# Kernel tuning notes

Measured on AMD Instinct MI355X. Metric: run time of the kernel, lower is better.

The kernel has to match this reference:

```python
import jax, jax.numpy as jnp
import numpy as np

U, I, H, E = 50000, 50000, 128, 800000


def segment_softmax(vals, seg, num):
    m = jax.ops.segment_max(vals, seg, num_segments=num)
    ex = jnp.exp(vals - m[seg])
    s = jax.ops.segment_sum(ex, seg, num_segments=num)
    return ex / s[seg]


def setup_inputs() -> dict:
    key = jax.random.key(0)
    ks = jax.random.split(key, 16)
    scale = 1.0 / np.sqrt(H)
    inp = {
        "u_emb": jax.random.normal(ks[0], (U, H), jnp.float32),
        "i_emb": jax.random.normal(ks[1], (I, H), jnp.float32),
        "pVui": jax.random.normal(ks[2], (E, H), jnp.float32),
        "pKiu": jax.random.normal(ks[3], (E, H), jnp.float32),
        "w1": jax.random.normal(ks[4], (H, H), jnp.float32) * scale,
        "w2": jax.random.normal(ks[5], (H, H), jnp.float32) * scale,
        "w1b": jax.random.normal(ks[6], (H, H), jnp.float32) * scale,
        "w2b": jax.random.normal(ks[7], (H, H), jnp.float32) * scale,
        "w3": jax.random.normal(ks[8], (H, H), jnp.float32) * scale,
        "w4": jax.random.normal(ks[9], (H, H), jnp.float32) * scale,
        "edge_index": jax.random.randint(ks[10], (2, E), 0, min(U, I), jnp.int64),
        "last_u": jax.random.randint(ks[11], (2, U), 0, I, jnp.int64),
        "last_i": jax.random.randint(ks[12], (2, I), 0, U, jnp.int64),
        "graph": jnp.zeros((1,), jnp.int64),
    }
    return inp


def reference(u_emb, i_emb, pVui, pKiu, w1, w2, w1b, w2b, w3, w4,
              edge_index, last_u, last_i, graph):
    sqrt_d = np.sqrt(float(u_emb.shape[1])).astype if False else float(np.sqrt(u_emb.shape[1]))
    nu, ni = u_emb.shape[0], i_emb.shape[0]
    src_u, dst_i = edge_index[0], edge_index[1]  # per-edge (user, item)

    # ---- longterm ----
    um_att = u_emb @ w2.T            # [U,H]
    im_att = i_emb @ w1.T            # [I,H]
    # sparse_dense_mul(edge_index, um_att @ im_att.T) -> per-edge dot products
    e_vals = jnp.sum(um_att[src_u] * im_att[dst_i], axis=-1)  # [E]
    e_ui = e_vals + jnp.sum(um_att[src_u] * pVui, axis=-1)
    alphas = segment_softmax(e_ui / sqrt_d, src_u, nu)        # softmax over items per user
    e_iu = e_vals + jnp.sum(im_att[dst_i] * pKiu, axis=-1)
    betas = segment_softmax(e_iu / sqrt_d, dst_i, ni)         # softmax over users per item
    um_b = u_emb @ w2b.T
    im_b = i_emb @ w1b.T
    hLu = jax.ops.segment_sum(alphas[:, None] * (im_b[dst_i] + pKiu), src_u, num_segments=nu)
    hLi = jax.ops.segment_sum(betas[:, None] * (um_b[src_u] + pVui), dst_i, num_segments=ni)

    # ---- shortterm ----
    last_item = i_emb[last_u[1]] @ w3.T   # [U,H] last item embedding per user
    last_user = u_emb[last_i[1]] @ w4.T   # [I,H] last user embedding per item
    a_vals = jnp.sum(last_item[src_u] * im_att[dst_i], axis=-1)
    s_alphas = segment_softmax(a_vals / sqrt_d, src_u, nu)
    b_vals = jnp.sum(last_user[src_u] * im_att[dst_i], axis=-1)
    s_betas = segment_softmax(b_vals / sqrt_d, dst_i, ni)
    # pass_messages with p = ones -> messages + 1
    hSu = jax.ops.segment_sum(s_alphas[:, None] * (im_att[dst_i] + 1.0), src_u, num_segments=nu)
    hSi = jax.ops.segment_sum(s_betas[:, None] * (um_att[src_u] + 1.0), dst_i, num_segments=ni)
    return (hLu, hSu, hLi, hSi)
```

## Files before the change

kernel.cpp:

```cpp
#include <hip/hip_runtime.h>
#include <hip/hip_bf16.h>
#include <math.h>


#define WB 1024

typedef float fvec4 __attribute__((ext_vector_type(4)));

__device__ __forceinline__ float4 nt_load4(const float* p) {
    fvec4 v = __builtin_nontemporal_load((const fvec4*)p);
    return make_float4(v.x, v.y, v.z, v.w);
}
__device__ __forceinline__ float dot4(float4 a, float4 b) {
    return a.x * b.x + a.y * b.y + a.z * b.z + a.w * b.w;
}

struct Gemm6Desc {
    const float* X[6];
    const float* W[6];
    float*       O[6];
    const int*   g[6];
    int          ostride[6];
    int          nrows[6];
};

__global__ __launch_bounds__(256) void gemm6_kernel(Gemm6Desc d)
{
    __shared__ float Xl[64 * 32];
    __shared__ float Wl[128 * 32];
    const int j6 = blockIdx.y;
    const float* __restrict__ X = d.X[j6];
    const float* __restrict__ W = d.W[j6];
    float* __restrict__ O       = d.O[j6];
    const int* __restrict__ gidx = d.g[j6];
    const int ostride = d.ostride[j6];
    const int nrows   = d.nrows[j6];

    const int t  = threadIdx.x;
    const int tx = t & 15;
    const int ty = t >> 4;
    const int brow = blockIdx.x * 64;
    if (brow >= nrows) return;

    float acc[4][8];
#pragma unroll
    for (int j = 0; j < 4; ++j)
#pragma unroll
        for (int i = 0; i < 8; ++i) acc[j][i] = 0.f;

    for (int k0 = 0; k0 < 128; k0 += 32) {
        __syncthreads();
#pragma unroll
        for (int u = 0; u < 2; ++u) {
            int idx4 = t + u * 256;
            int r  = idx4 >> 3;
            int k4 = idx4 & 7;
            int row = brow + r;
            float4 v = make_float4(0.f, 0.f, 0.f, 0.f);
            if (row < nrows) {
                int g = gidx ? gidx[row] : row;
                v = *(const float4*)(X + (size_t)g * 128 + k0 + k4 * 4);
            }
            int sw = k4 ^ ((r >> 3) & 7);
            *(float4*)(Xl + r * 32 + sw * 4) = v;
        }
#pragma unroll
        for (int u = 0; u < 4; ++u) {
            int idx4 = t + u * 256;
            int c  = idx4 >> 3;
            int k4 = idx4 & 7;
            float4 v = *(const float4*)(W + (size_t)c * 128 + k0 + k4 * 4);
            int sw = k4 ^ ((c >> 3) & 7);
            *(float4*)(Wl + c * 32 + sw * 4) = v;
        }
        __syncthreads();
#pragma unroll
        for (int k4 = 0; k4 < 8; ++k4) {
            float4 xv[4], wv[8];
#pragma unroll
            for (int j = 0; j < 4; ++j) {
                int r = ty * 4 + j;
                xv[j] = *(const float4*)(Xl + r * 32 + ((k4 ^ ((r >> 3) & 7)) * 4));
            }
#pragma unroll
            for (int i = 0; i < 8; ++i) {
                int c = tx * 8 + i;
                wv[i] = *(const float4*)(Wl + c * 32 + ((k4 ^ ((c >> 3) & 7)) * 4));
            }
#pragma unroll
            for (int j = 0; j < 4; ++j)
#pragma unroll
                for (int i = 0; i < 8; ++i) {
                    acc[j][i] += xv[j].x * wv[i].x;
                    acc[j][i] += xv[j].y * wv[i].y;
                    acc[j][i] += xv[j].z * wv[i].z;
                    acc[j][i] += xv[j].w * wv[i].w;
                }
        }
    }
#pragma unroll
    for (int j = 0; j < 4; ++j) {
        int row = brow + ty * 4 + j;
        if (row < nrows) {
            float* op = O + (size_t)row * ostride + tx * 8;
            *(float4*)(op)     = make_float4(acc[j][0], acc[j][1], acc[j][2], acc[j][3]);
            *(float4*)(op + 4) = make_float4(acc[j][4], acc[j][5], acc[j][6], acc[j][7]);
        }
    }
}

__global__ __launch_bounds__(256) void hist_kernel(
    const int* __restrict__ ei, int E,
    int* __restrict__ deg_u, int* __restrict__ deg_i)
{
    int e = blockIdx.x * 256 + threadIdx.x;
    if (e < E) {
        atomicAdd(&deg_u[ei[e]], 1);
        atomicAdd(&deg_i[ei[E + e]], 1);
    }
}

__global__ __launch_bounds__(256) void scan_blocksums_kernel(
    const int* __restrict__ deg_u, int nu, int nbu,
    const int* __restrict__ deg_i, int ni,
    int* __restrict__ bsum)
{
    int b = blockIdx.x;
    const int* deg; int n; int base;
    if (b < nbu) { deg = deg_u; n = nu; base = b * WB; }
    else         { deg = deg_i; n = ni; base = (b - nbu) * WB; }
    int t = threadIdx.x;
    int s = 0;
#pragma unroll
    for (int j = 0; j < 4; ++j) {
        int i = base + t * 4 + j;
        if (i < n) s += deg[i];
    }
#pragma unroll
    for (int o = 32; o > 0; o >>= 1) s += __shfl_xor(s, o);
    __shared__ int wt[4];
    if ((t & 63) == 0) wt[t >> 6] = s;
    __syncthreads();
    if (t == 0) bsum[b] = wt[0] + wt[1] + wt[2] + wt[3];
}

__global__ void scan_partials_kernel(
    const int* __restrict__ bsum, int* __restrict__ bscan,
    int nbu, int nbi,
    int* __restrict__ off_u, int nu, int* __restrict__ off_i, int ni)
{
    if (threadIdx.x != 0) return;
    if (blockIdx.x == 0) {
        int c = 0;
        for (int b = 0; b < nbu; ++b) { bscan[b] = c; c += bsum[b]; }
        off_u[nu] = c;
    } else {
        int c = 0;
        for (int b = 0; b < nbi; ++b) { bscan[nbu + b] = c; c += bsum[nbu + b]; }
        off_i[ni] = c;
    }
}

__global__ __launch_bounds__(256) void scan_final_kernel(
    const int* __restrict__ deg_u, int nu, int nbu,
    const int* __restrict__ deg_i, int ni,
    const int* __restrict__ bscan,
    int* __restrict__ off_u, int* __restrict__ cur_u,
    int* __restrict__ off_i, int* __restrict__ cur_i)
{
    int b = blockIdx.x;
    const int* deg; int n; int base; int* off; int* cur;
    if (b < nbu) { deg = deg_u; n = nu; base = b * WB; off = off_u; cur = cur_u; }
    else         { deg = deg_i; n = ni; base = (b - nbu) * WB; off = off_i; cur = cur_i; }
    int t = threadIdx.x;
    int lane = t & 63, w = t >> 6;
    int v[4];
    int s = 0;
#pragma unroll
    for (int j = 0; j < 4; ++j) {
        int i = base + t * 4 + j;
        v[j] = (i < n) ? deg[i] : 0;
        s += v[j];
    }
    int inc = s;
#pragma unroll
    for (int o = 1; o < 64; o <<= 1) {
        int x = __shfl_up(inc, o);
        if (lane >= o) inc += x;
    }
    int excl = inc - s;
    __shared__ int wt[4];
    if (lane == 63) wt[w] = inc;
    __syncthreads();
    int wbase = 0;
    for (int j = 0; j < w; ++j) wbase += wt[j];
    int e = bscan[b] + wbase + excl;
#pragma unroll
    for (int j = 0; j < 4; ++j) {
        int i = base + t * 4 + j;
        if (i < n) { off[i] = e; cur[i] = e; }
        e += v[j];
    }
}

__global__ __launch_bounds__(256) void scatter_ids_kernel(
    const int* __restrict__ ei, int E,
    int* __restrict__ cur_u, int* __restrict__ cur_i,
    int2* __restrict__ eu_list, int2* __restrict__ ei_list)
{
    int e = blockIdx.x * 256 + threadIdx.x;
    if (e < E) {
        int u = ei[e], v = ei[E + e];
        int pu = atomicAdd(&cur_u[u], 1);
        eu_list[pu] = make_int2(v, e);
        int pi = atomicAdd(&cur_i[v], 1);
        ei_list[pi] = make_int2(u, e);
    }
}

__global__ __launch_bounds__(256) void gather_u_kernel(
    const float* __restrict__ fusedU,
    const float* __restrict__ fusedI,
    const float* __restrict__ last_item, const float* __restrict__ last_user,
    const float* __restrict__ pVui, const float* __restrict__ pKiu,
    const int2* __restrict__ lst,
    const int* __restrict__ off_u,
    float2* __restrict__ x24,
    float* __restrict__ hLu, float* __restrict__ hSu, int U, float inv_sqrt_d)
{
    const int wid  = (int)(((size_t)blockIdx.x * blockDim.x + threadIdx.x) >> 6);
    const int lane = threadIdx.x & 63;
    if (wid >= U) return;
    const int g = lane >> 4;
    const int q = lane & 15;

    const float4* fu4 = (const float4*)(fusedU    + (size_t)wid * 256);
    const float4* li4 = (const float4*)(last_item + (size_t)wid * 128);
    const float4* lu4 = (const float4*)(last_user + (size_t)wid * 128);
    const float4 um0 = fu4[q],      um1 = fu4[q + 16];
    const float4 li0 = li4[q],      li1 = li4[q + 16];
    const float4 lu0 = lu4[q],      lu1 = lu4[q + 16];

    float4 a1l = make_float4(0.f,0.f,0.f,0.f), a1h = make_float4(0.f,0.f,0.f,0.f);
    float4 a3l = make_float4(0.f,0.f,0.f,0.f), a3h = make_float4(0.f,0.f,0.f,0.f);
    float s1 = 0.f, s3 = 0.f;
    const int e0 = off_u[wid], e1 = off_u[wid + 1];

    int eA = e0 + g, eB = eA + 4;
    bool vA = eA < e1, vB = eB < e1;
    int2 rA = vA ? lst[eA] : make_int2(0, 0);
    int2 rB = vB ? lst[eB] : rA;

    while (vA) {
        int eA2 = eA + 8, eB2 = eB + 8;
        bool vA2 = eA2 < e1, vB2 = eB2 < e1;
        int2 rA2 = vA2 ? lst[eA2] : make_int2(0, 0);
        int2 rB2 = vB2 ? lst[eB2] : rA2;

        const float4* fIA = (const float4*)(fusedI + (size_t)rA.x * 256);
        const float*  pvA = pVui + (size_t)rA.y * 128;
        const float*  pkA = pKiu + (size_t)rA.y * 128;
        const float4* fIB = (const float4*)(fusedI + (size_t)rB.x * 256);
        const float*  pvB = pVui + (size_t)rB.y * 128;
        const float*  pkB = pKiu + (size_t)rB.y * 128;

        float4 iaA0 = fIA[q],      iaA1 = fIA[q + 16];
        float4 ibA0 = fIA[32 + q], ibA1 = fIA[48 + q];
        float4 pvA0 = nt_load4(pvA + q * 4), pvA1 = nt_load4(pvA + 64 + q * 4);
        float4 pkA0 = nt_load4(pkA + q * 4), pkA1 = nt_load4(pkA + 64 + q * 4);
        float4 iaB0 = fIB[q],      iaB1 = fIB[q + 16];
        float4 ibB0 = fIB[32 + q], ibB1 = fIB[48 + q];
        float4 pvB0 = nt_load4(pvB + q * 4), pvB1 = nt_load4(pvB + 64 + q * 4);
        float4 pkB0 = nt_load4(pkB + q * 4), pkB1 = nt_load4(pkB + 64 + q * 4);

        float pA0 = dot4(um0, iaA0) + dot4(um1, iaA1);
        float qA1 = pA0 + dot4(um0, pvA0) + dot4(um1, pvA1);
        float qA2 = pA0 + dot4(iaA0, pkA0) + dot4(iaA1, pkA1);
        float qA3 = dot4(li0, iaA0) + dot4(li1, iaA1);
        float qA4 = dot4(lu0, iaA0) + dot4(lu1, iaA1);
        float pB0 = dot4(um0, iaB0) + dot4(um1, iaB1);
        float qB1 = pB0 + dot4(um0, pvB0) + dot4(um1, pvB1);
        float qB2 = pB0 + dot4(iaB0, pkB0) + dot4(iaB1, pkB1);
        float qB3 = dot4(li0, iaB0) + dot4(li1, iaB1);
        float qB4 = dot4(lu0, iaB0) + dot4(lu1, iaB1);
#pragma unroll
        for (int o = 8; o > 0; o >>= 1) {
            qA1 += __shfl_xor(qA1, o); qA2 += __shfl_xor(qA2, o);
            qA3 += __shfl_xor(qA3, o); qA4 += __shfl_xor(qA4, o);
            qB1 += __shfl_xor(qB1, o); qB2 += __shfl_xor(qB2, o);
            qB3 += __shfl_xor(qB3, o); qB4 += __shfl_xor(qB4, o);
        }
        float x1A = __expf(qA1 * inv_sqrt_d);
        float x2A = __expf(qA2 * inv_sqrt_d);
        float x3A = __expf(qA3 * inv_sqrt_d);
        float x4A = __expf(qA4 * inv_sqrt_d);
        float mB  = vB ? 1.f : 0.f;
        float x1B = __expf(qB1 * inv_sqrt_d) * mB;
        float x2B = __expf(qB2 * inv_sqrt_d);
        float x3B = __expf(qB3 * inv_sqrt_d) * mB;
        float x4B = __expf(qB4 * inv_sqrt_d);

        a1l.x += x1A*(ibA0.x+pkA0.x) + x1B*(ibB0.x+pkB0.x);
        a1l.y += x1A*(ibA0.y+pkA0.y) + x1B*(ibB0.y+pkB0.y);
        a1l.z += x1A*(ibA0.z+pkA0.z) + x1B*(ibB0.z+pkB0.z);
        a1l.w += x1A*(ibA0.w+pkA0.w) + x1B*(ibB0.w+pkB0.w);
        a1h.x += x1A*(ibA1.x+pkA1.x) + x1B*(ibB1.x+pkB1.x);
        a1h.y += x1A*(ibA1.y+pkA1.y) + x1B*(ibB1.y+pkB1.y);
        a1h.z += x1A*(ibA1.z+pkA1.z) + x1B*(ibB1.z+pkB1.z);
        a1h.w += x1A*(ibA1.w+pkA1.w) + x1B*(ibB1.w+pkB1.w);
        a3l.x += x3A*(iaA0.x+1.f) + x3B*(iaB0.x+1.f);
        a3l.y += x3A*(iaA0.y+1.f) + x3B*(iaB0.y+1.f);
        a3l.z += x3A*(iaA0.z+1.f) + x3B*(iaB0.z+1.f);
        a3l.w += x3A*(iaA0.w+1.f) + x3B*(iaB0.w+1.f);
        a3h.x += x3A*(iaA1.x+1.f) + x3B*(iaB1.x+1.f);
        a3h.y += x3A*(iaA1.y+1.f) + x3B*(iaB1.y+1.f);
        a3h.z += x3A*(iaA1.z+1.f) + x3B*(iaB1.z+1.f);
        a3h.w += x3A*(iaA1.w+1.f) + x3B*(iaB1.w+1.f);
        s1 += x1A + x1B; s3 += x3A + x3B;
        if (q == 0) {
            x24[rA.y] = make_float2(x2A, x4A);
            if (vB) x24[rB.y] = make_float2(x2B, x4B);
        }
        eA = eA2; eB = eB2; vA = vA2; vB = vB2; rA = rA2; rB = rB2;
    }
#pragma unroll
    for (int o = 16; o <= 32; o <<= 1) {
        a1l.x += __shfl_xor(a1l.x, o); a1l.y += __shfl_xor(a1l.y, o);
        a1l.z += __shfl_xor(a1l.z, o); a1l.w += __shfl_xor(a1l.w, o);
        a1h.x += __shfl_xor(a1h.x, o); a1h.y += __shfl_xor(a1h.y, o);
        a1h.z += __shfl_xor(a1h.z, o); a1h.w += __shfl_xor(a1h.w, o);
        a3l.x += __shfl_xor(a3l.x, o); a3l.y += __shfl_xor(a3l.y, o);
        a3l.z += __shfl_xor(a3l.z, o); a3l.w += __shfl_xor(a3l.w, o);
        a3h.x += __shfl_xor(a3h.x, o); a3h.y += __shfl_xor(a3h.y, o);
        a3h.z += __shfl_xor(a3h.z, o); a3h.w += __shfl_xor(a3h.w, o);
        s1 += __shfl_xor(s1, o);       s3 += __shfl_xor(s3, o);
    }
    if (lane < 16) {
        float r1 = (s1 > 0.f) ? 1.f / s1 : 0.f;
        float r3 = (s3 > 0.f) ? 1.f / s3 : 0.f;
        float4* oL = (float4*)(hLu + (size_t)wid * 128);
        float4* oS = (float4*)(hSu + (size_t)wid * 128);
        oL[q]      = make_float4(a1l.x*r1, a1l.y*r1, a1l.z*r1, a1l.w*r1);
        oL[q + 16] = make_float4(a1h.x*r1, a1h.y*r1, a1h.z*r1, a1h.w*r1);
        oS[q]      = make_float4(a3l.x*r3, a3l.y*r3, a3l.z*r3, a3l.w*r3);
        oS[q + 16] = make_float4(a3h.x*r3, a3h.y*r3, a3h.z*r3, a3h.w*r3);
    }
}

__global__ __launch_bounds__(256) void gather_i_kernel(
    const float* __restrict__ fusedU,
    const float* __restrict__ pVui,
    const int2* __restrict__ lst,
    const int* __restrict__ off_i,
    const float2* __restrict__ x24,
    float* __restrict__ hLi, float* __restrict__ hSi, int I)
{
    const int wid  = (int)(((size_t)blockIdx.x * blockDim.x + threadIdx.x) >> 6);
    const int lane = threadIdx.x & 63;
    if (wid >= I) return;
    const int g = lane >> 4;
    const int q = lane & 15;

    float4 a2l = make_float4(0.f,0.f,0.f,0.f), a2h = make_float4(0.f,0.f,0.f,0.f);
    float4 a4l = make_float4(0.f,0.f,0.f,0.f), a4h = make_float4(0.f,0.f,0.f,0.f);
    float s2 = 0.f, s4 = 0.f;
    const int e0 = off_i[wid], e1 = off_i[wid + 1];

    int eA = e0 + g, eB = eA + 4;
    bool vA = eA < e1, vB = eB < e1;
    int2 rA = vA ? lst[eA] : make_int2(0, 0);
    int2 rB = vB ? lst[eB] : rA;

    while (vA) {
        int eA2 = eA + 8, eB2 = eB + 8;
        bool vA2 = eA2 < e1, vB2 = eB2 < e1;
        int2 rA2 = vA2 ? lst[eA2] : make_int2(0, 0);
        int2 rB2 = vB2 ? lst[eB2] : rA2;

        const float4* fUA = (const float4*)(fusedU + (size_t)rA.x * 256);
        const float*  pvA = pVui + (size_t)rA.y * 128;
        const float4* fUB = (const float4*)(fusedU + (size_t)rB.x * 256);
        const float*  pvB = pVui + (size_t)rB.y * 128;

        float2 xA = x24[rA.y];
        float2 xB = x24[rB.y];
        float4 uaA0 = fUA[q],      uaA1 = fUA[q + 16];
        float4 ubA0 = fUA[32 + q], ubA1 = fUA[48 + q];
        float4 pvA0 = nt_load4(pvA + q * 4), pvA1 = nt_load4(pvA + 64 + q * 4);
        float4 uaB0 = fUB[q],      uaB1 = fUB[q + 16];
        float4 ubB0 = fUB[32 + q], ubB1 = fUB[48 + q];
        float4 pvB0 = nt_load4(pvB + q * 4), pvB1 = nt_load4(pvB + 64 + q * 4);

        if (!vB) { xB.x = 0.f; xB.y = 0.f; }
        a2l.x += xA.x*(ubA0.x+pvA0.x) + xB.x*(ubB0.x+pvB0.x);
        a2l.y += xA.x*(ubA0.y+pvA0.y) + xB.x*(ubB0.y+pvB0.y);
        a2l.z += xA.x*(ubA0.z+pvA0.z) + xB.x*(ubB0.z+pvB0.z);
        a2l.w += xA.x*(ubA0.w+pvA0.w) + xB.x*(ubB0.w+pvB0.w);
        a2h.x += xA.x*(ubA1.x+pvA1.x) + xB.x*(ubB1.x+pvB1.x);
        a2h.y += xA.x*(ubA1.y+pvA1.y) + xB.x*(ubB1.y+pvB1.y);
        a2h.z += xA.x*(ubA1.z+pvA1.z) + xB.x*(ubB1.z+pvB1.z);
        a2h.w += xA.x*(ubA1.w+pvA1.w) + xB.x*(ubB1.w+pvB1.w);
        a4l.x += xA.y*(uaA0.x+1.f) + xB.y*(uaB0.x+1.f);
        a4l.y += xA.y*(uaA0.y+1.f) + xB.y*(uaB0.y+1.f);
        a4l.z += xA.y*(uaA0.z+1.f) + xB.y*(uaB0.z+1.f);
        a4l.w += xA.y*(uaA0.w+1.f) + xB.y*(uaB0.w+1.f);
        a4h.x += xA.y*(uaA1.x+1.f) + xB.y*(uaB1.x+1.f);
        a4h.y += xA.y*(uaA1.y+1.f) + xB.y*(uaB1.y+1.f);
        a4h.z += xA.y*(uaA1.z+1.f) + xB.y*(uaB1.z+1.f);
        a4h.w += xA.y*(uaA1.w+1.f) + xB.y*(uaB1.w+1.f);
        s2 += xA.x + xB.x; s4 += xA.y + xB.y;

        eA = eA2; eB = eB2; vA = vA2; vB = vB2; rA = rA2; rB = rB2;
    }
#pragma unroll
    for (int o = 16; o <= 32; o <<= 1) {
        a2l.x += __shfl_xor(a2l.x, o); a2l.y += __shfl_xor(a2l.y, o);
        a2l.z += __shfl_xor(a2l.z, o); a2l.w += __shfl_xor(a2l.w, o);
        a2h.x += __shfl_xor(a2h.x, o); a2h.y += __shfl_xor(a2h.y, o);
        a2h.z += __shfl_xor(a2h.z, o); a2h.w += __shfl_xor(a2h.w, o);
        a4l.x += __shfl_xor(a4l.x, o); a4l.y += __shfl_xor(a4l.y, o);
        a4l.z += __shfl_xor(a4l.z, o); a4l.w += __shfl_xor(a4l.w, o);
        a4h.x += __shfl_xor(a4h.x, o); a4h.y += __shfl_xor(a4h.y, o);
        a4h.z += __shfl_xor(a4h.w - a4h.w + a4h.z, o); a4h.w += __shfl_xor(a4h.w, o);
        s2 += __shfl_xor(s2, o);       s4 += __shfl_xor(s4, o);
    }
    if (lane < 16) {
        float r2 = (s2 > 0.f) ? 1.f / s2 : 0.f;
        float r4 = (s4 > 0.f) ? 1.f / s4 : 0.f;
        float4* oL = (float4*)(hLi + (size_t)wid * 128);
        float4* oS = (float4*)(hSi + (size_t)wid * 128);
        oL[q]      = make_float4(a2l.x*r2, a2l.y*r2, a2l.z*r2, a2l.w*r2);
        oL[q + 16] = make_float4(a2h.x*r2, a2h.y*r2, a2h.z*r2, a2h.w*r2);
        oS[q]      = make_float4(a4l.x*r4, a4l.y*r4, a4l.z*r4, a4l.w*r4);
        oS[q + 16] = make_float4(a4h.x*r4, a4h.y*r4, a4h.z*r4, a4h.w*r4);
    }
}

extern "C" void kernel_launch(void* const* d_in, const int* in_sizes, int n_in,
                              void* d_out, int out_size, void* d_ws, size_t ws_size,
                              hipStream_t stream)
{
    const float* u_emb = (const float*)d_in[0];
    const float* i_emb = (const float*)d_in[1];
    const float* pVui  = (const float*)d_in[2];
    const float* pKiu  = (const float*)d_in[3];
    const float* w1    = (const float*)d_in[4];
    const float* w2    = (const float*)d_in[5];
    const float* w1b   = (const float*)d_in[6];
    const float* w2b   = (const float*)d_in[7];
    const float* w3    = (const float*)d_in[8];
    const float* w4    = (const float*)d_in[9];
    const int* edge_index = (const int*)d_in[10];
    const int* last_u     = (const int*)d_in[11];
    const int* last_i     = (const int*)d_in[12];

    const int U = in_sizes[0] / 128;
    const int I = in_sizes[1] / 128;
    const int E = in_sizes[10] / 2;
    const int nbu = (U + WB - 1) / WB;
    const int nbi = (I + WB - 1) / WB;

    float* ws = (float*)d_ws;
    float* fusedU    = ws;  ws += (size_t)U * 256;
    float* fusedI    = ws;  ws += (size_t)I * 256;
    float* last_item = ws;  ws += (size_t)U * 128;
    float* last_user = ws;  ws += (size_t)I * 128;
    float2* x24 = (float2*)ws;  ws += (size_t)E * 2;
    int2* eu_list = (int2*)ws;  ws += (size_t)E * 2;
    int2* ei_list = (int2*)ws;  ws += (size_t)E * 2;
    int* ip = (int*)ws;
    int* deg_u   = ip;  ip += U;
    int* deg_i   = ip;  ip += I;
    int* off_u   = ip;  ip += U + 1;
    int* off_i   = ip;  ip += I + 1;
    int* cur_u   = ip;  ip += U;
    int* cur_i   = ip;  ip += I;
    int* bsum    = ip;  ip += nbu + nbi;
    int* bscan   = ip;  ip += nbu + nbi;

    float* hLu = (float*)d_out;
    float* hSu = hLu + (size_t)U * 128;
    float* hLi = hSu + (size_t)U * 128;
    float* hSi = hLi + (size_t)I * 128;

    hipMemsetAsync(deg_u, 0, (size_t)(U + I) * sizeof(int), stream);

    dim3 blk(256);
    const int eblk = (E + 255) / 256;
    hist_kernel<<<eblk, blk, 0, stream>>>(edge_index, E, deg_u, deg_i);
    scan_blocksums_kernel<<<nbu + nbi, blk, 0, stream>>>(deg_u, U, nbu, deg_i, I, bsum);
    scan_partials_kernel<<<2, 64, 0, stream>>>(bsum, bscan, nbu, nbi, off_u, U, off_i, I);
    scan_final_kernel<<<nbu + nbi, blk, 0, stream>>>(
        deg_u, U, nbu, deg_i, I, bscan, off_u, cur_u, off_i, cur_i);
    scatter_ids_kernel<<<eblk, blk, 0, stream>>>(edge_index, E, cur_u, cur_i, eu_list, ei_list);

    Gemm6Desc gd;
    gd.X[0] = u_emb; gd.W[0] = w2;  gd.O[0] = fusedU;       gd.g[0] = nullptr;    gd.ostride[0] = 256; gd.nrows[0] = U;
    gd.X[1] = u_emb; gd.W[1] = w2b; gd.O[1] = fusedU + 128; gd.g[1] = nullptr;    gd.ostride[1] = 256; gd.nrows[1] = U;
    gd.X[2] = i_emb; gd.W[2] = w1;  gd.O[2] = fusedI;       gd.g[2] = nullptr;    gd.ostride[2] = 256; gd.nrows[2] = I;
    gd.X[3] = i_emb; gd.W[3] = w1b; gd.O[3] = fusedI + 128; gd.g[3] = nullptr;    gd.ostride[3] = 256; gd.nrows[3] = I;
    gd.X[4] = i_emb; gd.W[4] = w3;  gd.O[4] = last_item;    gd.g[4] = last_u + U; gd.ostride[4] = 128; gd.nrows[4] = U;
    gd.X[5] = u_emb; gd.W[5] = w4;  gd.O[5] = last_user;    gd.g[5] = last_i + I; gd.ostride[5] = 128; gd.nrows[5] = I;
    int maxrows = (U > I) ? U : I;
    dim3 ggrid((maxrows + 63) / 64, 6);
    gemm6_kernel<<<ggrid, blk, 0, stream>>>(gd);

    const float inv_sqrt_d = 1.0f / sqrtf(128.0f);
    gather_u_kernel<<<(U + 3) / 4, blk, 0, stream>>>(
        fusedU, fusedI, last_item, last_user, pVui, pKiu, eu_list,
        off_u, x24, hLu, hSu, U, inv_sqrt_d);
    gather_i_kernel<<<(I + 3) / 4, blk, 0, stream>>>(
        fusedU, pVui, ei_list, off_i, x24, hLi, hSi, I);
}
```

Baseline: 838.4 us.

## Store projected embeddings as bf16 and map one node per quarter-wave

The GEMM outputs (fusedU, fusedI, last_item, last_user) are now stored as bf16 with round-to-nearest-even and widened back to fp32 in the gather kernels. This halves the bytes of the randomly gathered node rows. The gather kernels also change from one wave per node with four edge lanes to one 16-lane group per node, each processing two edges per step. That removes the cross-group shuffle reduction and lets the x24 loads in the item kernel be prefetched. The cost is reduced precision in the intermediate projections, plus more serial work per node for high-degree nodes.

```diff
diff --git a/kernel.cpp b/kernel.cpp
--- a/kernel.cpp
+++ b/kernel.cpp
@@ -14,11 +14,25 @@
 __device__ __forceinline__ float dot4(float4 a, float4 b) {
     return a.x * b.x + a.y * b.y + a.z * b.z + a.w * b.w;
 }
+__device__ __forceinline__ void bfu(uint4 v, float4& lo, float4& hi) {
+    lo.x = __uint_as_float(v.x << 16);
+    lo.y = __uint_as_float(v.x & 0xFFFF0000u);
+    lo.z = __uint_as_float(v.y << 16);
+    lo.w = __uint_as_float(v.y & 0xFFFF0000u);
+    hi.x = __uint_as_float(v.z << 16);
+    hi.y = __uint_as_float(v.z & 0xFFFF0000u);
+    hi.z = __uint_as_float(v.w << 16);
+    hi.w = __uint_as_float(v.w & 0xFFFF0000u);
+}
+__device__ __forceinline__ unsigned rne16(float f) {
+    unsigned u = __float_as_uint(f);
+    return (u + 0x7FFFu + ((u >> 16) & 1u)) >> 16;
+}
 
 struct Gemm6Desc {
     const float* X[6];
     const float* W[6];
-    float*       O[6];
+    unsigned short* O[6];
     const int*   g[6];
     int          ostride[6];
     int          nrows[6];
@@ -31,7 +45,7 @@
     const int j6 = blockIdx.y;
     const float* __restrict__ X = d.X[j6];
     const float* __restrict__ W = d.W[j6];
-    float* __restrict__ O       = d.O[j6];
+    unsigned short* __restrict__ O = d.O[j6];
     const int* __restrict__ gidx = d.g[j6];
     const int ostride = d.ostride[j6];
     const int nrows   = d.nrows[j6];
@@ -102,9 +116,13 @@
     for (int j = 0; j < 4; ++j) {
         int row = brow + ty * 4 + j;
         if (row < nrows) {
-            float* op = O + (size_t)row * ostride + tx * 8;
-            *(float4*)(op)     = make_float4(acc[j][0], acc[j][1], acc[j][2], acc[j][3]);
-            *(float4*)(op + 4) = make_float4(acc[j][4], acc[j][5], acc[j][6], acc[j][7]);
+            unsigned short* op = O + (size_t)row * ostride + tx * 8;
+            uint4 p;
+            p.x = rne16(acc[j][0]) | (rne16(acc[j][1]) << 16);
+            p.y = rne16(acc[j][2]) | (rne16(acc[j][3]) << 16);
+            p.z = rne16(acc[j][4]) | (rne16(acc[j][5]) << 16);
+            p.w = rne16(acc[j][6]) | (rne16(acc[j][7]) << 16);
+            *(uint4*)op = p;
         }
     }
 }
@@ -219,68 +237,69 @@
 }
 
 __global__ __launch_bounds__(256) void gather_u_kernel(
-    const float* __restrict__ fusedU,
-    const float* __restrict__ fusedI,
-    const float* __restrict__ last_item, const float* __restrict__ last_user,
+    const unsigned short* __restrict__ fusedU,
+    const unsigned short* __restrict__ fusedI,
+    const unsigned short* __restrict__ last_item,
+    const unsigned short* __restrict__ last_user,
     const float* __restrict__ pVui, const float* __restrict__ pKiu,
-    const int2* __restrict__ lst,
-    const int* __restrict__ off_u,
+    const int2* __restrict__ lst, const int* __restrict__ off_u,
     float2* __restrict__ x24,
     float* __restrict__ hLu, float* __restrict__ hSu, int U, float inv_sqrt_d)
 {
-    const int wid  = (int)(((size_t)blockIdx.x * blockDim.x + threadIdx.x) >> 6);
+    const int wv   = (int)(((size_t)blockIdx.x * blockDim.x + threadIdx.x) >> 6);
     const int lane = threadIdx.x & 63;
-    if (wid >= U) return;
     const int g = lane >> 4;
     const int q = lane & 15;
-
-    const float4* fu4 = (const float4*)(fusedU    + (size_t)wid * 256);
-    const float4* li4 = (const float4*)(last_item + (size_t)wid * 128);
-    const float4* lu4 = (const float4*)(last_user + (size_t)wid * 128);
-    const float4 um0 = fu4[q],      um1 = fu4[q + 16];
-    const float4 li0 = li4[q],      li1 = li4[q + 16];
-    const float4 lu0 = lu4[q],      lu1 = lu4[q + 16];
+    const int uid = wv * 4 + g;
+    if (uid >= U) return;
+
+    float4 um0, um1, li0, li1, lu0, lu1;
+    bfu(((const uint4*)(fusedU    + (size_t)uid * 256))[q], um0, um1);
+    bfu(((const uint4*)(last_item + (size_t)uid * 128))[q], li0, li1);
+    bfu(((const uint4*)(last_user + (size_t)uid * 128))[q], lu0, lu1);
 
     float4 a1l = make_float4(0.f,0.f,0.f,0.f), a1h = make_float4(0.f,0.f,0.f,0.f);
     float4 a3l = make_float4(0.f,0.f,0.f,0.f), a3h = make_float4(0.f,0.f,0.f,0.f);
     float s1 = 0.f, s3 = 0.f;
-    const int e0 = off_u[wid], e1 = off_u[wid + 1];
-
-    int eA = e0 + g, eB = eA + 4;
+    const int e0 = off_u[uid], e1 = off_u[uid + 1];
+
+    int eA = e0, eB = e0 + 1;
     bool vA = eA < e1, vB = eB < e1;
     int2 rA = vA ? lst[eA] : make_int2(0, 0);
     int2 rB = vB ? lst[eB] : rA;
 
     while (vA) {
-        int eA2 = eA + 8, eB2 = eB + 8;
+        int eA2 = eA + 2, eB2 = eB + 2;
         bool vA2 = eA2 < e1, vB2 = eB2 < e1;
         int2 rA2 = vA2 ? lst[eA2] : make_int2(0, 0);
         int2 rB2 = vB2 ? lst[eB2] : rA2;
 
-        const float4* fIA = (const float4*)(fusedI + (size_t)rA.x * 256);
-        const float*  pvA = pVui + (size_t)rA.y * 128;
-        const float*  pkA = pKiu + (size_t)rA.y * 128;
-        const float4* fIB = (const float4*)(fusedI + (size_t)rB.x * 256);
-        const float*  pvB = pVui + (size_t)rB.y * 128;
-        const float*  pkB = pKiu + (size_t)rB.y * 128;
-
-        float4 iaA0 = fIA[q],      iaA1 = fIA[q + 16];
-        float4 ibA0 = fIA[32 + q], ibA1 = fIA[48 + q];
-        float4 pvA0 = nt_load4(pvA + q * 4), pvA1 = nt_load4(pvA + 64 + q * 4);
-        float4 pkA0 = nt_load4(pkA + q * 4), pkA1 = nt_load4(pkA + 64 + q * 4);
-        float4 iaB0 = fIB[q],      iaB1 = fIB[q + 16];
-        float4 ibB0 = fIB[32 + q], ibB1 = fIB[48 + q];
-        float4 pvB0 = nt_load4(pvB + q * 4), pvB1 = nt_load4(pvB + 64 + q * 4);
-        float4 pkB0 = nt_load4(pkB + q * 4), pkB1 = nt_load4(pkB + 64 + q * 4);
-
-        float pA0 = dot4(um0, iaA0) + dot4(um1, iaA1);
-        float qA1 = pA0 + dot4(um0, pvA0) + dot4(um1, pvA1);
-        float qA2 = pA0 + dot4(iaA0, pkA0) + dot4(iaA1, pkA1);
+        const uint4* fIA = (const uint4*)(fusedI + (size_t)rA.x * 256);
+        const float* pvA = pVui + (size_t)rA.y * 128 + q * 8;
+        const float* pkA = pKiu + (size_t)rA.y * 128 + q * 8;
+        const uint4* fIB = (const uint4*)(fusedI + (size_t)rB.x * 256);
+        const float* pvB = pVui + (size_t)rB.y * 128 + q * 8;
+        const float* pkB = pKiu + (size_t)rB.y * 128 + q * 8;
+
+        uint4 iaAp = fIA[q], ibAp = fIA[16 + q];
+        uint4 iaBp = fIB[q], ibBp = fIB[16 + q];
+        float4 pvA0 = nt_load4(pvA), pvA1 = nt_load4(pvA + 4);
+        float4 pkA0 = nt_load4(pkA), pkA1 = nt_load4(pkA + 4);
+        float4 pvB0 = nt_load4(pvB), pvB1 = nt_load4(pvB + 4);
+        float4 pkB0 = nt_load4(pkB), pkB1 = nt_load4(pkB + 4);
+
+        float4 iaA0, iaA1, ibA0, ibA1, iaB0, iaB1, ibB0, ibB1;
+        bfu(iaAp, iaA0, iaA1); bfu(ibAp, ibA0, ibA1);
+        bfu(iaBp, iaB0, iaB1); bfu(ibBp, ibB0, ibB1);
+
+        float dA0 = dot4(um0, iaA0) + dot4(um1, iaA1);
+        float qA1 = dA0 + dot4(um0, pvA0) + dot4(um1, pvA1);
+        float qA2 = dA0 + dot4(iaA0, pkA0) + dot4(iaA1, pkA1);
         float qA3 = dot4(li0, iaA0) + dot4(li1, iaA1);
         float qA4 = dot4(lu0, iaA0) + dot4(lu1, iaA1);
-        float pB0 = dot4(um0, iaB0) + dot4(um1, iaB1);
-        float qB1 = pB0 + dot4(um0, pvB0) + dot4(um1, pvB1);
-        float qB2 = pB0 + dot4(iaB0, pkB0) + dot4(iaB1, pkB1);
+        float dB0 = dot4(um0, iaB0) + dot4(um1, iaB1);
+        float qB1 = dB0 + dot4(um0, pvB0) + dot4(um1, pvB1);
+        float qB2 = dB0 + dot4(iaB0, pkB0) + dot4(iaB1, pkB1);
         float qB3 = dot4(li0, iaB0) + dot4(li1, iaB1);
         float qB4 = dot4(lu0, iaB0) + dot4(lu1, iaB1);
 #pragma unroll
@@ -323,73 +342,63 @@
         }
         eA = eA2; eB = eB2; vA = vA2; vB = vB2; rA = rA2; rB = rB2;
     }
-#pragma unroll
-    for (int o = 16; o <= 32; o <<= 1) {
-        a1l.x += __shfl_xor(a1l.x, o); a1l.y += __shfl_xor(a1l.y, o);
-        a1l.z += __shfl_xor(a1l.z, o); a1l.w += __shfl_xor(a1l.w, o);
-        a1h.x += __shfl_xor(a1h.x, o); a1h.y += __shfl_xor(a1h.y, o);
-        a1h.z += __shfl_xor(a1h.z, o); a1h.w += __shfl_xor(a1h.w, o);
-        a3l.x += __shfl_xor(a3l.x, o); a3l.y += __shfl_xor(a3l.y, o);
-        a3l.z += __shfl_xor(a3l.z, o); a3l.w += __shfl_xor(a3l.w, o);
-        a3h.x += __shfl_xor(a3h.x, o); a3h.y += __shfl_xor(a3h.y, o);
-        a3h.z += __shfl_xor(a3h.z, o); a3h.w += __shfl_xor(a3h.w, o);
-        s1 += __shfl_xor(s1, o);       s3 += __shfl_xor(s3, o);
-    }
-    if (lane < 16) {
-        float r1 = (s1 > 0.f) ? 1.f / s1 : 0.f;
-        float r3 = (s3 > 0.f) ? 1.f / s3 : 0.f;
-        float4* oL = (float4*)(hLu + (size_t)wid * 128);
-        float4* oS = (float4*)(hSu + (size_t)wid * 128);
-        oL[q]      = make_float4(a1l.x*r1, a1l.y*r1, a1l.z*r1, a1l.w*r1);
-        oL[q + 16] = make_float4(a1h.x*r1, a1h.y*r1, a1h.z*r1, a1h.w*r1);
-        oS[q]      = make_float4(a3l.x*r3, a3l.y*r3, a3l.z*r3, a3l.w*r3);
-        oS[q + 16] = make_float4(a3h.x*r3, a3h.y*r3, a3h.z*r3, a3h.w*r3);
-    }
+    float r1 = (s1 > 0.f) ? 1.f / s1 : 0.f;
+    float r3 = (s3 > 0.f) ? 1.f / s3 : 0.f;
+    float4* oL = (float4*)(hLu + (size_t)uid * 128);
+    float4* oS = (float4*)(hSu + (size_t)uid * 128);
+    oL[2*q]     = make_float4(a1l.x*r1, a1l.y*r1, a1l.z*r1, a1l.w*r1);
+    oL[2*q + 1] = make_float4(a1h.x*r1, a1h.y*r1, a1h.z*r1, a1h.w*r1);
+    oS[2*q]     = make_float4(a3l.x*r3, a3l.y*r3, a3l.z*r3, a3l.w*r3);
+    oS[2*q + 1] = make_float4(a3h.x*r3, a3h.y*r3, a3h.z*r3, a3h.w*r3);
 }
 
 __global__ __launch_bounds__(256) void gather_i_kernel(
-    const float* __restrict__ fusedU,
+    const unsigned short* __restrict__ fusedU,
     const float* __restrict__ pVui,
-    const int2* __restrict__ lst,
-    const int* __restrict__ off_i,
+    const int2* __restrict__ lst, const int* __restrict__ off_i,
     const float2* __restrict__ x24,
     float* __restrict__ hLi, float* __restrict__ hSi, int I)
 {
-    const int wid  = (int)(((size_t)blockIdx.x * blockDim.x + threadIdx.x) >> 6);
+    const int wv   = (int)(((size_t)blockIdx.x * blockDim.x + threadIdx.x) >> 6);
     const int lane = threadIdx.x & 63;
-    if (wid >= I) return;
     const int g = lane >> 4;
     const int q = lane & 15;
+    const int iid = wv * 4 + g;
+    if (iid >= I) return;
 
     float4 a2l = make_float4(0.f,0.f,0.f,0.f), a2h = make_float4(0.f,0.f,0.f,0.f);
     float4 a4l = make_float4(0.f,0.f,0.f,0.f), a4h = make_float4(0.f,0.f,0.f,0.f);
     float s2 = 0.f, s4 = 0.f;
-    const int e0 = off_i[wid], e1 = off_i[wid + 1];
-
-    int eA = e0 + g, eB = eA + 4;
+    const int e0 = off_i[iid], e1 = off_i[iid + 1];
+
+    int eA = e0, eB = e0 + 1;
     bool vA = eA < e1, vB = eB < e1;
     int2 rA = vA ? lst[eA] : make_int2(0, 0);
     int2 rB = vB ? lst[eB] : rA;
+    float2 xA = vA ? x24[rA.y] : make_float2(0.f, 0.f);
+    float2 xB = vB ? x24[rB.y] : make_float2(0.f, 0.f);
 
     while (vA) {
-        int eA2 = eA + 8, eB2 = eB + 8;
+        int eA2 = eA + 2, eB2 = eB + 2;
         bool vA2 = eA2 < e1, vB2 = eB2 < e1;
         int2 rA2 = vA2 ? lst[eA2] : make_int2(0, 0);
         int2 rB2 = vB2 ? lst[eB2] : rA2;
-
-        const float4* fUA = (const float4*)(fusedU + (size_t)rA.x * 256);
-        const float*  pvA = pVui + (size_t)rA.y * 128;
-        const float4* fUB = (const float4*)(fusedU + (size_t)rB.x * 256);
-        const float*  pvB = pVui + (size_t)rB.y * 128;
-
-        float2 xA = x24[rA.y];
-        float2 xB = x24[rB.y];
-        float4 uaA0 = fUA[q],      uaA1 = fUA[q + 16];
-        float4 ubA0 = fUA[32 + q], ubA1 = fUA[48 + q];
-        float4 pvA0 = nt_load4(pvA + q * 4), pvA1 = nt_load4(pvA + 64 + q * 4);
-        float4 uaB0 = fUB[q],      uaB1 = fUB[q + 16];
-        float4 ubB0 = fUB[32 + q], ubB1 = fUB[48 + q];
-        float4 pvB0 = nt_load4(pvB + q * 4), pvB1 = nt_load4(pvB + 64 + q * 4);
+        float2 xA2v = vA2 ? x24[rA2.y] : make_float2(0.f, 0.f);
+        float2 xB2v = vB2 ? x24[rB2.y] : make_float2(0.f, 0.f);
+
+        const uint4* fUA = (const uint4*)(fusedU + (size_t)rA.x * 256);
+        const float* pvA = pVui + (size_t)rA.y * 128 + q * 8;
+        const uint4* fUB = (const uint4*)(fusedU + (size_t)rB.x * 256);
+        const float* pvB = pVui + (size_t)rB.y * 128 + q * 8;
+
+        uint4 uaAp = fUA[q], ubAp = fUA[16 + q];
+        uint4 uaBp = fUB[q], ubBp = fUB[16 + q];
+        float4 pvA0 = nt_load4(pvA), pvA1 = nt_load4(pvA + 4);
+        float4 pvB0 = nt_load4(pvB), pvB1 = nt_load4(pvB + 4);
+
+        float4 uaA0, uaA1, ubA0, ubA1, uaB0, uaB1, ubB0, ubB1;
+        bfu(uaAp, uaA0, uaA1); bfu(ubAp, ubA0, ubA1);
+        bfu(uaBp, uaB0, uaB1); bfu(ubBp, ubB0, ubB1);
 
         if (!vB) { xB.x = 0.f; xB.y = 0.f; }
         a2l.x += xA.x*(ubA0.x+pvA0.x) + xB.x*(ubB0.x+pvB0.x);
@@ -410,30 +419,17 @@
         a4h.w += xA.y*(uaA1.w+1.f) + xB.y*(uaB1.w+1.f);
         s2 += xA.x + xB.x; s4 += xA.y + xB.y;
 
-        eA = eA2; eB = eB2; vA = vA2; vB = vB2; rA = rA2; rB = rB2;
-    }
-#pragma unroll
-    for (int o = 16; o <= 32; o <<= 1) {
-        a2l.x += __shfl_xor(a2l.x, o); a2l.y += __shfl_xor(a2l.y, o);
-        a2l.z += __shfl_xor(a2l.z, o); a2l.w += __shfl_xor(a2l.w, o);
-        a2h.x += __shfl_xor(a2h.x, o); a2h.y += __shfl_xor(a2h.y, o);
-        a2h.z += __shfl_xor(a2h.z, o); a2h.w += __shfl_xor(a2h.w, o);
-        a4l.x += __shfl_xor(a4l.x, o); a4l.y += __shfl_xor(a4l.y, o);
-        a4l.z += __shfl_xor(a4l.z, o); a4l.w += __shfl_xor(a4l.w, o);
-        a4h.x += __shfl_xor(a4h.x, o); a4h.y += __shfl_xor(a4h.y, o);
-        a4h.z += __shfl_xor(a4h.w - a4h.w + a4h.z, o); a4h.w += __shfl_xor(a4h.w, o);
-        s2 += __shfl_xor(s2, o);       s4 += __shfl_xor(s4, o);
-    }
-    if (lane < 16) {
-        float r2 = (s2 > 0.f) ? 1.f / s2 : 0.f;
-        float r4 = (s4 > 0.f) ? 1.f / s4 : 0.f;
-        float4* oL = (float4*)(hLi + (size_t)wid * 128);
-        float4* oS = (float4*)(hSi + (size_t)wid * 128);
-        oL[q]      = make_float4(a2l.x*r2, a2l.y*r2, a2l.z*r2, a2l.w*r2);
-        oL[q + 16] = make_float4(a2h.x*r2, a2h.y*r2, a2h.z*r2, a2h.w*r2);
-        oS[q]      = make_float4(a4l.x*r4, a4l.y*r4, a4l.z*r4, a4l.w*r4);
-        oS[q + 16] = make_float4(a4h.x*r4, a4h.y*r4, a4h.z*r4, a4h.w*r4);
-    }
+        eA = eA2; eB = eB2; vA = vA2; vB = vB2;
+        rA = rA2; rB = rB2; xA = xA2v; xB = xB2v;
+    }
+    float r2 = (s2 > 0.f) ? 1.f / s2 : 0.f;
+    float r4 = (s4 > 0.f) ? 1.f / s4 : 0.f;
+    float4* oL = (float4*)(hLi + (size_t)iid * 128);
+    float4* oS = (float4*)(hSi + (size_t)iid * 128);
+    oL[2*q]     = make_float4(a2l.x*r2, a2l.y*r2, a2l.z*r2, a2l.w*r2);
+    oL[2*q + 1] = make_float4(a2h.x*r2, a2h.y*r2, a2h.z*r2, a2h.w*r2);
+    oS[2*q]     = make_float4(a4l.x*r4, a4l.y*r4, a4l.z*r4, a4l.w*r4);
+    oS[2*q + 1] = make_float4(a4h.x*r4, a4h.y*r4, a4h.z*r4, a4h.w*r4);
 }
 
 extern "C" void kernel_launch(void* const* d_in, const int* in_sizes, int n_in,
@@ -460,11 +456,12 @@
     const int nbu = (U + WB - 1) / WB;
     const int nbi = (I + WB - 1) / WB;
 
-    float* ws = (float*)d_ws;
-    float* fusedU    = ws;  ws += (size_t)U * 256;
-    float* fusedI    = ws;  ws += (size_t)I * 256;
-    float* last_item = ws;  ws += (size_t)U * 128;
-    float* last_user = ws;  ws += (size_t)I * 128;
+    unsigned short* us = (unsigned short*)d_ws;
+    unsigned short* fusedU    = us;  us += (size_t)U * 256;
+    unsigned short* fusedI    = us;  us += (size_t)I * 256;
+    unsigned short* last_item = us;  us += (size_t)U * 128;
+    unsigned short* last_user = us;  us += (size_t)I * 128;
+    float* ws = (float*)us;
     float2* x24 = (float2*)ws;  ws += (size_t)E * 2;
     int2* eu_list = (int2*)ws;  ws += (size_t)E * 2;
     int2* ei_list = (int2*)ws;  ws += (size_t)E * 2;
@@ -492,7 +489,8 @@
     scan_partials_kernel<<<2, 64, 0, stream>>>(bsum, bscan, nbu, nbi, off_u, U, off_i, I);
     scan_final_kernel<<<nbu + nbi, blk, 0, stream>>>(
         deg_u, U, nbu, deg_i, I, bscan, off_u, cur_u, off_i, cur_i);
-    scatter_ids_kernel<<<eblk, blk, 0, stream>>>(edge_index, E, cur_u, cur_i, eu_list, ei_list);
+    scatter_ids_kernel<<<eblk, blk, 0, stream>>>(
+        edge_index, E, cur_u, cur_i, eu_list, ei_list);
 
     Gemm6Desc gd;
     gd.X[0] = u_emb; gd.W[0] = w2;  gd.O[0] = fusedU;       gd.g[0] = nullptr;    gd.ostride[0] = 256; gd.nrows[0] = U;
@@ -506,9 +504,9 @@
     gemm6_kernel<<<ggrid, blk, 0, stream>>>(gd);
 
     const float inv_sqrt_d = 1.0f / sqrtf(128.0f);
-    gather_u_kernel<<<(U + 3) / 4, blk, 0, stream>>>(
-        fusedU, fusedI, last_item, last_user, pVui, pKiu, eu_list,
-        off_u, x24, hLu, hSu, U, inv_sqrt_d);
-    gather_i_kernel<<<(I + 3) / 4, blk, 0, stream>>>(
+    gather_u_kernel<<<(U + 15) / 16, blk, 0, stream>>>(
+        fusedU, fusedI, last_item, last_user, pVui, pKiu, eu_list, off_u,
+        x24, hLu, hSu, U, inv_sqrt_d);
+    gather_i_kernel<<<(I + 15) / 16, blk, 0, stream>>>(
         fusedU, pVui, ei_list, off_i, x24, hLi, hSi, I);
 }
```

Result: faster. 819.8 us (-2.2%).
